# Kernel tuning notes

Hardware: AMD Instinct MI355X
Metric: run time of the kernel (lower is better)

## Reference

```python
import jax, jax.numpy as jnp
import numpy as np
from jax import lax

B, S, D = 8, 1024, 128

def setup_inputs() -> dict:
    key = jax.random.key(0)
    ks = jax.random.split(key, 6)
    scale = 1.0 / np.sqrt(D)
    return {
        "x": jax.random.normal(ks[0], (B, S, D), dtype=jnp.float32),
        "Wk": jax.random.normal(ks[1], (D, D), dtype=jnp.float32) * scale,
        "Wv": jax.random.normal(ks[2], (D, D), dtype=jnp.float32) * scale,
        "Wq": jax.random.normal(ks[3], (D, D), dtype=jnp.float32) * scale,
        "Wg": jax.random.normal(ks[4], (D, 3), dtype=jnp.float32) * scale,
        "bg": jnp.zeros((3,), dtype=jnp.float32),
    }

def reference(x, Wk, Wv, Wq, Wg, bg):
    b, s, d = x.shape
    k = x @ Wk  # [b,s,d]
    v = x @ Wv
    q = x @ Wq
    gates = jax.nn.sigmoid(x @ Wg + bg)  # [b,s,3]
    alpha, eta, theta = gates[..., 0], gates[..., 1], gates[..., 2]  # [b,s]

    M0 = jnp.zeros((b, d, d), dtype=x.dtype)
    S0 = jnp.zeros((b, d, d), dtype=x.dtype)

    # time-major scan inputs
    xs = (jnp.swapaxes(k, 0, 1), jnp.swapaxes(v, 0, 1), jnp.swapaxes(q, 0, 1),
          jnp.swapaxes(alpha, 0, 1), jnp.swapaxes(eta, 0, 1), jnp.swapaxes(theta, 0, 1))

    def scan_fn(carry, inp):
        M_prev, S_prev = carry
        kt, vt, qt, at, et, tt = inp  # kt/vt/qt: [b,d]; at/et/tt: [b]
        # NOTE: original einsum 'bd,bdd->bd' takes the DIAGONAL of M (faithful)
        diagM = jnp.einsum('bdd->bd', M_prev)  # [b,d]
        yt = qt * diagM
        pred = kt * diagM
        error = pred - vt
        grad = kt[:, :, None] * error[:, None, :]  # outer product [b,d,d]
        S_new = et[:, None, None] * S_prev - tt[:, None, None] * grad
        M_new = (1.0 - at[:, None, None]) * M_prev + S_new
        return (M_new, S_new), yt

    (M_final, S_final), outputs = lax.scan(scan_fn, (M0, S0), xs)
    outputs = jnp.swapaxes(outputs, 0, 1)  # [b,s,d]
    return (outputs, (M_final, S_final))
```

## Files before the change

### kernel.cpp

```cpp
#include <hip/hip_runtime.h>
#include <math.h>

#define NB 8
#define NS 1024
#define ND 128
#define NC 64
#define NL 16

#define OFF_K  0u
#define OFF_Q  1048576u
#define OFF_V  2097152u
#define OFF_E  3145728u
#define OFF_GA 4194304u
#define OFF_GE 4202496u
#define OFF_GT 4210688u
#define OFF_W  4218880u
#define OFF_C  4227072u
#define OFF_P  4235264u

#define PL_A00 (OFF_P)
#define PL_A01 (OFF_P +  65536u)
#define PL_A10 (OFF_P + 131072u)
#define PL_A11 (OFF_P + 196608u)
#define PL_B0  (OFF_P + 262144u)
#define PL_B1  (OFF_P + 327680u)
#define PL_MST (OFF_P + 393216u)
#define PL_SST (OFF_P + 458752u)
#define PL_WCA (OFF_P + 524288u)
#define PL_WCB (OFF_P + 524800u)
#define PL_WCD (OFF_P + 525312u)
#define PL_WRQ (OFF_P + 525824u)
#define PL_WRP (OFF_P + 526336u)
#define PL_WRA (OFF_P + 526848u)
#define OFF_WT (OFF_P + 532480u)
#define WT_LO  49152u

typedef short bf16x8 __attribute__((ext_vector_type(8)));
typedef float f32x4  __attribute__((ext_vector_type(4)));

static __device__ __forceinline__ unsigned short f2bf(float f) {
    unsigned u = __builtin_bit_cast(unsigned, f);
    unsigned r = (u + 0x7FFFu + ((u >> 16) & 1u)) >> 16;
    return (unsigned short)r;
}
static __device__ __forceinline__ float bf2f(unsigned short h) {
    unsigned u = ((unsigned)h) << 16;
    return __builtin_bit_cast(float, u);
}
static __device__ __forceinline__ void split2(float a, float b,
                                              unsigned& hi, unsigned& lo) {
    unsigned short ah = f2bf(a), bh = f2bf(b);
    float ar = a - bf2f(ah), br = b - bf2f(bh);
    hi = (unsigned)ah | ((unsigned)bh << 16);
    lo = (unsigned)f2bf(ar) | ((unsigned)f2bf(br) << 16);
}

__global__ __launch_bounds__(256) void wtprep_kernel(
    const float* __restrict__ Wk, const float* __restrict__ Wv,
    const float* __restrict__ Wq, unsigned short* __restrict__ wtg,
    float* __restrict__ outMS)
{
    const int m    = blockIdx.x >> 4;
    const int cgrp = blockIdx.x & 15;
    const int tid  = threadIdx.x;
    const int cl   = tid >> 5;
    const int h    = tid & 31;
    const int c    = cgrp * 8 + cl;
    const float* W = (m == 0) ? Wk : (m == 1) ? Wv : Wq;

    float f[4];
#pragma unroll
    for (int i = 0; i < 4; ++i)
        f[i] = W[(h * 4 + i) * ND + c];
    uint2 hi, lo;
    split2(f[0], f[1], hi.x, lo.x);
    split2(f[2], f[3], hi.y, lo.y);
    const unsigned base = (unsigned)m * 16384u + (unsigned)c * 128u + (unsigned)h * 4u;
    *(uint2*)&wtg[base]         = hi;
    *(uint2*)&wtg[WT_LO + base] = lo;

    const int gidx = blockIdx.x * 256 + tid;
    const float4 z = {0.f, 0.f, 0.f, 0.f};
#pragma unroll
    for (int l = 0; l < 6; ++l) {
        int i4 = gidx + l * 12288;
        if (i4 < 65536) ((float4*)outMS)[i4] = z;
    }
}

__global__ __launch_bounds__(256) void proj_mfma(
    const float* __restrict__ x, const unsigned short* __restrict__ wtg,
    const float* __restrict__ Wg, const float* __restrict__ bg,
    float* __restrict__ Kb, float* __restrict__ Vb, float* __restrict__ Qb,
    float* __restrict__ ga, float* __restrict__ ge, float* __restrict__ gt)
{
    __shared__ unsigned short xs_hi[32 * 136];
    __shared__ unsigned short xs_lo[32 * 136];
    __shared__ unsigned short wt_hi[64 * 136];
    __shared__ unsigned short wt_lo[64 * 136];

    const int tid  = threadIdx.x;
    const int bid  = blockIdx.x;
    const int m    = bid >> 9;
    const int rt   = (bid >> 1) & 255;
    const int ch   = bid & 1;
    const int row0 = rt * 32;

    const float4* x4 = (const float4*)x;
#pragma unroll
    for (int l = 0; l < 4; ++l) {
        int idx = tid + l * 256;
        int r = idx >> 5, kq = idx & 31;
        float4 f = x4[(row0 + r) * 32 + kq];
        uint2 hi, lo;
        split2(f.x, f.y, hi.x, lo.x);
        split2(f.z, f.w, hi.y, lo.y);
        *(uint2*)&xs_hi[r * 136 + kq * 4] = hi;
        *(uint2*)&xs_lo[r * 136 + kq * 4] = lo;
    }
    const uint4* wh4 = (const uint4*)(wtg + m * 16384 + ch * 64 * 128);
    const uint4* wl4 = (const uint4*)(wtg + WT_LO + m * 16384 + ch * 64 * 128);
#pragma unroll
    for (int l = 0; l < 4; ++l) {
        int idx = tid + l * 256;
        int c = idx >> 4, u = idx & 15;
        *(uint4*)&wt_hi[c * 136 + u * 8] = wh4[c * 16 + u];
        *(uint4*)&wt_lo[c * 136 + u * 8] = wl4[c * 16 + u];
    }
    __syncthreads();

    const int wid  = tid >> 6;
    const int lane = tid & 63;
    const int rg   = wid >> 1;
    const int cg   = wid & 1;
    const int lrow = rg * 16 + (lane & 15);
    const int quad = lane >> 4;

    f32x4 acc[2];
    acc[0] = (f32x4){0.f, 0.f, 0.f, 0.f};
    acc[1] = (f32x4){0.f, 0.f, 0.f, 0.f};

#pragma unroll
    for (int kk = 0; kk < 4; ++kk) {
        bf16x8 ah = *(const bf16x8*)&xs_hi[lrow * 136 + kk * 32 + quad * 8];
        bf16x8 al = *(const bf16x8*)&xs_lo[lrow * 136 + kk * 32 + quad * 8];
#pragma unroll
        for (int ct = 0; ct < 2; ++ct) {
            int cl = cg * 32 + ct * 16 + (lane & 15);
            bf16x8 bh = *(const bf16x8*)&wt_hi[cl * 136 + kk * 32 + quad * 8];
            bf16x8 bl = *(const bf16x8*)&wt_lo[cl * 136 + kk * 32 + quad * 8];
            acc[ct] = __builtin_amdgcn_mfma_f32_16x16x32_bf16(ah, bh, acc[ct], 0, 0, 0);
            acc[ct] = __builtin_amdgcn_mfma_f32_16x16x32_bf16(ah, bl, acc[ct], 0, 0, 0);
            acc[ct] = __builtin_amdgcn_mfma_f32_16x16x32_bf16(al, bh, acc[ct], 0, 0, 0);
        }
    }

    float* dst = (m == 0) ? Kb : (m == 1) ? Vb : Qb;
#pragma unroll
    for (int ct = 0; ct < 2; ++ct) {
        int ocol = ch * 64 + cg * 32 + ct * 16 + (lane & 15);
#pragma unroll
        for (int r4 = 0; r4 < 4; ++r4) {
            int orow = row0 + rg * 16 + quad * 4 + r4;
            dst[orow * ND + ocol] = acc[ct][r4];
        }
    }

    if (m == 0 && ch == 0 && tid < 96) {
        int r = tid / 3, j = tid % 3;
        float z = bg[j];
        const float* xr = x + (row0 + r) * ND;
#pragma unroll 4
        for (int i = 0; i < ND; ++i)
            z = fmaf(xr[i], Wg[i * 3 + j], z);
        float gate = 1.0f / (1.0f + expf(-z));
        int row = row0 + r;
        float* gd = (j == 0) ? ga : (j == 1) ? ge : gt;
        gd[row] = gate;
    }
}

__global__ __launch_bounds__(128) void scan_phase1(
    const float* __restrict__ Kb, const float* __restrict__ Vb,
    const float* __restrict__ ga, const float* __restrict__ ge,
    const float* __restrict__ gt, float* __restrict__ ws)
{
    __shared__ float la[NL], le[NL], lt[NL];
    const int tid = threadIdx.x;
    const int b   = blockIdx.x >> 6;
    const int c   = blockIdx.x & 63;
    const int t0  = c * NL;
    const int g0  = b * NS + t0;

    if (tid < 16)       la[tid]      = ga[g0 + tid];
    else if (tid < 32)  le[tid - 16] = ge[g0 + tid - 16];
    else if (tid < 48)  lt[tid - 32] = gt[g0 + tid - 32];
    __syncthreads();

    const int d = tid;
    float A00 = 1.f, A01 = 0.f, A10 = 0.f, A11 = 1.f, B0 = 0.f, B1 = 0.f;
    int base = g0 * ND + d;
#pragma unroll
    for (int t = 0; t < NL; ++t) {
        float k = Kb[base], v = Vb[base];
        float a = la[t], e = le[t], th = lt[t];
        float tk = th * k;
        float gg = -tk * k;
        float h  = tk * v;
        float p  = (1.0f - a) + gg;
        float u0 = e * A10;
        float u1 = e * A11;
        float u2 = fmaf(e, B1, h);
        float n00 = fmaf(p, A00, u0), n10 = fmaf(gg, A00, u0);
        float n01 = fmaf(p, A01, u1), n11 = fmaf(gg, A01, u1);
        float nb0 = fmaf(p, B0, u2),  nb1 = fmaf(gg, B0, u2);
        A00 = n00; A01 = n01; A10 = n10; A11 = n11; B0 = nb0; B1 = nb1;
        base += ND;
    }
    const int pidx = (b * NC + c) * ND + d;
    ws[PL_A00 + pidx] = A00;
    ws[PL_A01 + pidx] = A01;
    ws[PL_A10 + pidx] = A10;
    ws[PL_A11 + pidx] = A11;
    ws[PL_B0  + pidx] = B0;
    ws[PL_B1  + pidx] = B1;

    if (tid == 0) {
        float al = 1.f, be = 1.f, de = 0.f;
#pragma unroll
        for (int t = NL - 1; t >= 0; --t) {
            float e1 = le[t];
            float o1 = 1.0f - la[t];
            de = fmaf(e1, de, o1 * be);
            al *= e1;
            be *= o1;
        }
        ws[PL_WCA + b * NC + c] = al;
        ws[PL_WCB + b * NC + c] = be;
        ws[PL_WCD + b * NC + c] = de;
    }
}

__global__ __launch_bounds__(64) void scan_phase2(float* __restrict__ ws)
{
    const int tid = threadIdx.x;
    if (blockIdx.x < 16) {
        const int b = blockIdx.x >> 1;
        const int d = (blockIdx.x & 1) * 64 + tid;
        float m = 0.f, s = 0.f;
        int idx = (b * NC) * ND + d;
#pragma unroll 4
        for (int c = 0; c < NC; ++c) {
            ws[PL_MST + idx] = m;
            ws[PL_SST + idx] = s;
            float A00 = ws[PL_A00 + idx], A01 = ws[PL_A01 + idx];
            float A10 = ws[PL_A10 + idx], A11 = ws[PL_A11 + idx];
            float B0  = ws[PL_B0  + idx], B1  = ws[PL_B1  + idx];
            float nm = fmaf(A00, m, fmaf(A01, s, B0));
            float ns = fmaf(A10, m, fmaf(A11, s, B1));
            m = nm; s = ns;
            idx += ND;
        }
    } else if (tid < 8) {
        const int b = tid;
        float Qp = 1.f, P = 1.f, A = 1.f;
        for (int c = NC - 1; c >= 0; --c) {
            ws[PL_WRQ + b * NC + c] = Qp;
            ws[PL_WRP + b * NC + c] = P;
            ws[PL_WRA + b * NC + c] = A;
            float al = ws[PL_WCA + b * NC + c];
            float be = ws[PL_WCB + b * NC + c];
            float de = ws[PL_WCD + b * NC + c];
            float nA = fmaf(al, A, de * P);
            Qp *= al; P *= be; A = nA;
        }
    }
}

__global__ __launch_bounds__(128) void scan_phase3(
    const float* __restrict__ Kb, const float* __restrict__ Vb,
    const float* __restrict__ Qb,
    const float* __restrict__ ga, const float* __restrict__ ge,
    const float* __restrict__ gt,
    float* __restrict__ out, float* __restrict__ errb,
    float* __restrict__ wb,  float* __restrict__ cb,
    float* __restrict__ ws)
{
    __shared__ float la[NL], le[NL], lt[NL];
    const int tid = threadIdx.x;
    const int b   = blockIdx.x >> 6;
    const int c   = blockIdx.x & 63;
    const int t0  = c * NL;
    const int g0  = b * NS + t0;

    if (tid < 16)       la[tid]      = ga[g0 + tid];
    else if (tid < 32)  le[tid - 16] = ge[g0 + tid - 16];
    else if (tid < 48)  lt[tid - 32] = gt[g0 + tid - 32];
    __syncthreads();

    const int d = tid;
    const int pidx = (b * NC + c) * ND + d;
    float m = ws[PL_MST + pidx];
    float s = ws[PL_SST + pidx];
    int base = g0 * ND + d;
#pragma unroll
    for (int t = 0; t < NL; ++t) {
        float k = Kb[base], v = Vb[base], q = Qb[base];
        float a = la[t], e = le[t], th = lt[t];
        float err = fmaf(k, m, -v);
        out[base]  = q * m;
        errb[base] = err;
        float tk = th * k;
        float u  = fmaf(-(tk * k), m, tk * v);
        s = fmaf(e, s, u);
        m = fmaf(1.0f - a, m, s);
        base += ND;
    }

    if (tid == 0) {
        float Qp = ws[PL_WRQ + b * NC + c];
        float P  = ws[PL_WRP + b * NC + c];
        float A  = ws[PL_WRA + b * NC + c];
#pragma unroll
        for (int t = NL - 1; t >= 0; --t) {
            wb[g0 + t] = -lt[t] * Qp;
            cb[g0 + t] = -lt[t] * A;
            float e1 = le[t];
            float o1 = 1.0f - la[t];
            Qp *= e1;
            P  *= o1;
            A   = fmaf(e1, A, P);
        }
    }
}

__global__ __launch_bounds__(256) void finalgemm_kernel(
    const float* __restrict__ Kb, const float* __restrict__ errb,
    const float* __restrict__ wb, const float* __restrict__ cb,
    float* __restrict__ outMS)
{
    __shared__ float ks[64 * 16];
    __shared__ float wcs[64 * 2];
    const int tid = threadIdx.x;
    const int bid = blockIdx.x;
    const int b   = bid >> 7;
    const int tc  = (bid >> 3) & 15;
    const int rg  = bid & 7;
    const int bt0 = b * NS + tc * 64;

    {
        int tl = tid >> 2, r4 = tid & 3;
        *(float4*)&ks[tl * 16 + r4 * 4] =
            *(const float4*)&Kb[(bt0 + tl) * ND + rg * 16 + r4 * 4];
    }
    if (tid < 64) {
        wcs[tid * 2]     = wb[bt0 + tid];
        wcs[tid * 2 + 1] = cb[bt0 + tid];
    }
    __syncthreads();

    const int j = tid & 127;
    const int h = tid >> 7;
    float accM[8], accS[8];
#pragma unroll
    for (int i = 0; i < 8; ++i) { accM[i] = 0.f; accS[i] = 0.f; }

    int ebase = bt0 * ND + j;
#pragma unroll 4
    for (int t = 0; t < 64; ++t) {
        float ej = errb[ebase];
        float2 wc = *(const float2*)&wcs[t * 2];
        float wej = wc.x * ej, cej = wc.y * ej;
        float4 k0 = *(const float4*)&ks[t * 16 + h * 8];
        float4 k1 = *(const float4*)&ks[t * 16 + h * 8 + 4];
        accS[0] = fmaf(k0.x, wej, accS[0]); accM[0] = fmaf(k0.x, cej, accM[0]);
        accS[1] = fmaf(k0.y, wej, accS[1]); accM[1] = fmaf(k0.y, cej, accM[1]);
        accS[2] = fmaf(k0.z, wej, accS[2]); accM[2] = fmaf(k0.z, cej, accM[2]);
        accS[3] = fmaf(k0.w, wej, accS[3]); accM[3] = fmaf(k0.w, cej, accM[3]);
        accS[4] = fmaf(k1.x, wej, accS[4]); accM[4] = fmaf(k1.x, cej, accM[4]);
        accS[5] = fmaf(k1.y, wej, accS[5]); accM[5] = fmaf(k1.y, cej, accM[5]);
        accS[6] = fmaf(k1.z, wej, accS[6]); accM[6] = fmaf(k1.z, cej, accM[6]);
        accS[7] = fmaf(k1.w, wej, accS[7]); accM[7] = fmaf(k1.w, cej, accM[7]);
        ebase += ND;
    }

    const int robase = rg * 16 + h * 8;
#pragma unroll
    for (int i = 0; i < 8; ++i) {
        int off = b * (ND * ND) + (robase + i) * ND + j;
        atomicAdd(&outMS[off], accM[i]);
        atomicAdd(&outMS[131072u + off], accS[i]);
    }
}

extern "C" void kernel_launch(void* const* d_in, const int* in_sizes, int n_in,
                              void* d_out, int out_size, void* d_ws, size_t ws_size,
                              hipStream_t stream) {
    const float* x  = (const float*)d_in[0];
    const float* Wk = (const float*)d_in[1];
    const float* Wv = (const float*)d_in[2];
    const float* Wq = (const float*)d_in[3];
    const float* Wg = (const float*)d_in[4];
    const float* bg = (const float*)d_in[5];
    float* out = (float*)d_out;
    float* ws  = (float*)d_ws;

    float* Kb  = ws + OFF_K;
    float* Qb  = ws + OFF_Q;
    float* Vb  = ws + OFF_V;
    float* Eb  = ws + OFF_E;
    float* ga  = ws + OFF_GA;
    float* ge  = ws + OFF_GE;
    float* gt  = ws + OFF_GT;
    float* wbf = ws + OFF_W;
    float* cbf = ws + OFF_C;
    float* outMS = out + 1048576u;
    unsigned short* wtg = (unsigned short*)(ws + OFF_WT);

    wtprep_kernel<<<48, 256, 0, stream>>>(Wk, Wv, Wq, wtg, outMS);
    proj_mfma<<<1536, 256, 0, stream>>>(x, wtg, Wg, bg,
                                        Kb, Vb, Qb, ga, ge, gt);
    scan_phase1<<<NB * NC, 128, 0, stream>>>(Kb, Vb, ga, ge, gt, ws);
    scan_phase2<<<17, 64, 0, stream>>>(ws);
    scan_phase3<<<NB * NC, 128, 0, stream>>>(Kb, Vb, Qb, ga, ge, gt,
                                             out, Eb, wbf, cbf, ws);
    finalgemm_kernel<<<1024, 256, 0, stream>>>(Kb, Eb, wbf, cbf, outMS);
}
```

Before: 117.2 us.

## Fuse three scan phases into one cooperative kernel with grid syncs

Merges the chunk-summary, cross-chunk prefix, and chunk-replay scan kernels into a single cooperative launch separated by grid-wide syncs. K, V and Q for each chunk are loaded into registers once and reused in both the summary and replay passes, so the second global read is gone. This removes two kernel launches and the reload of K/V. In exchange it adds two grid barriers, and the middle phase runs on only 9 of 512 blocks while the others wait. The 48 extra registers per thread may also reduce occupancy.

Result: slower. 242.4 us (+106.8%).

```diff
diff --git a/kernel.cpp b/kernel.cpp
--- a/kernel.cpp
+++ b/kernel.cpp
@@ -1,5 +1,8 @@
 #include <hip/hip_runtime.h>
+#include <hip/hip_cooperative_groups.h>
 #include <math.h>
+
+namespace cg = cooperative_groups;
 
 #define NB 8
 #define NS 1024
@@ -180,11 +183,17 @@
     }
 }
 
-__global__ __launch_bounds__(128) void scan_phase1(
+__global__ __launch_bounds__(128) void scan_fused(
     const float* __restrict__ Kb, const float* __restrict__ Vb,
+    const float* __restrict__ Qb,
     const float* __restrict__ ga, const float* __restrict__ ge,
-    const float* __restrict__ gt, float* __restrict__ ws)
+    const float* __restrict__ gt,
+    float* __restrict__ out, float* __restrict__ errb,
+    float* __restrict__ wb,  float* __restrict__ cb,
+    float* __restrict__ ws)
 {
+    cg::grid_group grid = cg::this_grid();
+
     __shared__ float la[NL], le[NL], lt[NL];
     const int tid = threadIdx.x;
     const int b   = blockIdx.x >> 6;
@@ -195,62 +204,69 @@
     if (tid < 16)       la[tid]      = ga[g0 + tid];
     else if (tid < 32)  le[tid - 16] = ge[g0 + tid - 16];
     else if (tid < 48)  lt[tid - 32] = gt[g0 + tid - 32];
+
+    float k[NL], v[NL], q[NL];
+    {
+        int base = g0 * ND + tid;
+#pragma unroll
+        for (int t = 0; t < NL; ++t) {
+            k[t] = Kb[base];
+            v[t] = Vb[base];
+            q[t] = Qb[base];
+            base += ND;
+        }
+    }
     __syncthreads();
 
-    const int d = tid;
-    float A00 = 1.f, A01 = 0.f, A10 = 0.f, A11 = 1.f, B0 = 0.f, B1 = 0.f;
-    int base = g0 * ND + d;
-#pragma unroll
-    for (int t = 0; t < NL; ++t) {
-        float k = Kb[base], v = Vb[base];
-        float a = la[t], e = le[t], th = lt[t];
-        float tk = th * k;
-        float gg = -tk * k;
-        float h  = tk * v;
-        float p  = (1.0f - a) + gg;
-        float u0 = e * A10;
-        float u1 = e * A11;
-        float u2 = fmaf(e, B1, h);
-        float n00 = fmaf(p, A00, u0), n10 = fmaf(gg, A00, u0);
-        float n01 = fmaf(p, A01, u1), n11 = fmaf(gg, A01, u1);
-        float nb0 = fmaf(p, B0, u2),  nb1 = fmaf(gg, B0, u2);
-        A00 = n00; A01 = n01; A10 = n10; A11 = n11; B0 = nb0; B1 = nb1;
-        base += ND;
-    }
-    const int pidx = (b * NC + c) * ND + d;
-    ws[PL_A00 + pidx] = A00;
-    ws[PL_A01 + pidx] = A01;
-    ws[PL_A10 + pidx] = A10;
-    ws[PL_A11 + pidx] = A11;
-    ws[PL_B0  + pidx] = B0;
-    ws[PL_B1  + pidx] = B1;
-
-    if (tid == 0) {
-        float al = 1.f, be = 1.f, de = 0.f;
-#pragma unroll
-        for (int t = NL - 1; t >= 0; --t) {
-            float e1 = le[t];
-            float o1 = 1.0f - la[t];
-            de = fmaf(e1, de, o1 * be);
-            al *= e1;
-            be *= o1;
-        }
-        ws[PL_WCA + b * NC + c] = al;
-        ws[PL_WCB + b * NC + c] = be;
-        ws[PL_WCD + b * NC + c] = de;
-    }
-}
-
-__global__ __launch_bounds__(64) void scan_phase2(float* __restrict__ ws)
-{
-    const int tid = threadIdx.x;
-    if (blockIdx.x < 16) {
-        const int b = blockIdx.x >> 1;
-        const int d = (blockIdx.x & 1) * 64 + tid;
+    {
+        float A00 = 1.f, A01 = 0.f, A10 = 0.f, A11 = 1.f, B0 = 0.f, B1 = 0.f;
+#pragma unroll
+        for (int t = 0; t < NL; ++t) {
+            float a = la[t], e = le[t], th = lt[t];
+            float tk = th * k[t];
+            float gg = -tk * k[t];
+            float h  = tk * v[t];
+            float p  = (1.0f - a) + gg;
+            float u0 = e * A10;
+            float u1 = e * A11;
+            float u2 = fmaf(e, B1, h);
+            float n00 = fmaf(p, A00, u0), n10 = fmaf(gg, A00, u0);
+            float n01 = fmaf(p, A01, u1), n11 = fmaf(gg, A01, u1);
+            float nb0 = fmaf(p, B0, u2),  nb1 = fmaf(gg, B0, u2);
+            A00 = n00; A01 = n01; A10 = n10; A11 = n11; B0 = nb0; B1 = nb1;
+        }
+        const int pidx = (b * NC + c) * ND + tid;
+        ws[PL_A00 + pidx] = A00;
+        ws[PL_A01 + pidx] = A01;
+        ws[PL_A10 + pidx] = A10;
+        ws[PL_A11 + pidx] = A11;
+        ws[PL_B0  + pidx] = B0;
+        ws[PL_B1  + pidx] = B1;
+
+        if (tid == 0) {
+            float al = 1.f, be = 1.f, de = 0.f;
+#pragma unroll
+            for (int t = NL - 1; t >= 0; --t) {
+                float e1 = le[t];
+                float o1 = 1.0f - la[t];
+                de = fmaf(e1, de, o1 * be);
+                al *= e1;
+                be *= o1;
+            }
+            ws[PL_WCA + b * NC + c] = al;
+            ws[PL_WCB + b * NC + c] = be;
+            ws[PL_WCD + b * NC + c] = de;
+        }
+    }
+
+    grid.sync();
+
+    if (blockIdx.x < 8) {
+        const int pb = blockIdx.x;
         float m = 0.f, s = 0.f;
-        int idx = (b * NC) * ND + d;
+        int idx = (pb * NC) * ND + tid;
 #pragma unroll 4
-        for (int c = 0; c < NC; ++c) {
+        for (int cc = 0; cc < NC; ++cc) {
             ws[PL_MST + idx] = m;
             ws[PL_SST + idx] = s;
             float A00 = ws[PL_A00 + idx], A01 = ws[PL_A01 + idx];
@@ -261,75 +277,55 @@
             m = nm; s = ns;
             idx += ND;
         }
-    } else if (tid < 8) {
-        const int b = tid;
+    } else if (blockIdx.x == 8 && tid < 8) {
+        const int pb = tid;
         float Qp = 1.f, P = 1.f, A = 1.f;
-        for (int c = NC - 1; c >= 0; --c) {
-            ws[PL_WRQ + b * NC + c] = Qp;
-            ws[PL_WRP + b * NC + c] = P;
-            ws[PL_WRA + b * NC + c] = A;
-            float al = ws[PL_WCA + b * NC + c];
-            float be = ws[PL_WCB + b * NC + c];
-            float de = ws[PL_WCD + b * NC + c];
+        for (int cc = NC - 1; cc >= 0; --cc) {
+            ws[PL_WRQ + pb * NC + cc] = Qp;
+            ws[PL_WRP + pb * NC + cc] = P;
+            ws[PL_WRA + pb * NC + cc] = A;
+            float al = ws[PL_WCA + pb * NC + cc];
+            float be = ws[PL_WCB + pb * NC + cc];
+            float de = ws[PL_WCD + pb * NC + cc];
             float nA = fmaf(al, A, de * P);
             Qp *= al; P *= be; A = nA;
         }
     }
-}
-
-__global__ __launch_bounds__(128) void scan_phase3(
-    const float* __restrict__ Kb, const float* __restrict__ Vb,
-    const float* __restrict__ Qb,
-    const float* __restrict__ ga, const float* __restrict__ ge,
-    const float* __restrict__ gt,
-    float* __restrict__ out, float* __restrict__ errb,
-    float* __restrict__ wb,  float* __restrict__ cb,
-    float* __restrict__ ws)
-{
-    __shared__ float la[NL], le[NL], lt[NL];
-    const int tid = threadIdx.x;
-    const int b   = blockIdx.x >> 6;
-    const int c   = blockIdx.x & 63;
-    const int t0  = c * NL;
-    const int g0  = b * NS + t0;
-
-    if (tid < 16)       la[tid]      = ga[g0 + tid];
-    else if (tid < 32)  le[tid - 16] = ge[g0 + tid - 16];
-    else if (tid < 48)  lt[tid - 32] = gt[g0 + tid - 32];
-    __syncthreads();
-
-    const int d = tid;
-    const int pidx = (b * NC + c) * ND + d;
-    float m = ws[PL_MST + pidx];
-    float s = ws[PL_SST + pidx];
-    int base = g0 * ND + d;
-#pragma unroll
-    for (int t = 0; t < NL; ++t) {
-        float k = Kb[base], v = Vb[base], q = Qb[base];
-        float a = la[t], e = le[t], th = lt[t];
-        float err = fmaf(k, m, -v);
-        out[base]  = q * m;
-        errb[base] = err;
-        float tk = th * k;
-        float u  = fmaf(-(tk * k), m, tk * v);
-        s = fmaf(e, s, u);
-        m = fmaf(1.0f - a, m, s);
-        base += ND;
-    }
-
-    if (tid == 0) {
-        float Qp = ws[PL_WRQ + b * NC + c];
-        float P  = ws[PL_WRP + b * NC + c];
-        float A  = ws[PL_WRA + b * NC + c];
-#pragma unroll
-        for (int t = NL - 1; t >= 0; --t) {
-            wb[g0 + t] = -lt[t] * Qp;
-            cb[g0 + t] = -lt[t] * A;
-            float e1 = le[t];
-            float o1 = 1.0f - la[t];
-            Qp *= e1;
-            P  *= o1;
-            A   = fmaf(e1, A, P);
+
+    grid.sync();
+
+    {
+        const int pidx = (b * NC + c) * ND + tid;
+        float m = ws[PL_MST + pidx];
+        float s = ws[PL_SST + pidx];
+        int base = g0 * ND + tid;
+#pragma unroll
+        for (int t = 0; t < NL; ++t) {
+            float a = la[t], e = le[t], th = lt[t];
+            float err = fmaf(k[t], m, -v[t]);
+            out[base]  = q[t] * m;
+            errb[base] = err;
+            float tk = th * k[t];
+            float u  = fmaf(-(tk * k[t]), m, tk * v[t]);
+            s = fmaf(e, s, u);
+            m = fmaf(1.0f - a, m, s);
+            base += ND;
+        }
+
+        if (tid == 0) {
+            float Qp = ws[PL_WRQ + b * NC + c];
+            float P  = ws[PL_WRP + b * NC + c];
+            float A  = ws[PL_WRA + b * NC + c];
+#pragma unroll
+            for (int t = NL - 1; t >= 0; --t) {
+                wb[g0 + t] = -lt[t] * Qp;
+                cb[g0 + t] = -lt[t] * A;
+                float e1 = le[t];
+                float o1 = 1.0f - la[t];
+                Qp *= e1;
+                P  *= o1;
+                A   = fmaf(e1, A, P);
+            }
         }
     }
 }
@@ -420,9 +416,13 @@
     wtprep_kernel<<<48, 256, 0, stream>>>(Wk, Wv, Wq, wtg, outMS);
     proj_mfma<<<1536, 256, 0, stream>>>(x, wtg, Wg, bg,
                                         Kb, Vb, Qb, ga, ge, gt);
-    scan_phase1<<<NB * NC, 128, 0, stream>>>(Kb, Vb, ga, ge, gt, ws);
-    scan_phase2<<<17, 64, 0, stream>>>(ws);
-    scan_phase3<<<NB * NC, 128, 0, stream>>>(Kb, Vb, Qb, ga, ge, gt,
-                                             out, Eb, wbf, cbf, ws);
+
+    void* sargs[] = {(void*)&Kb, (void*)&Vb, (void*)&Qb,
+                     (void*)&ga, (void*)&ge, (void*)&gt,
+                     (void*)&out, (void*)&Eb, (void*)&wbf, (void*)&cbf,
+                     (void*)&ws};
+    hipLaunchCooperativeKernel((void*)scan_fused, dim3(NB * NC), dim3(128),
+                               sargs, 0, stream);
+
     finalgemm_kernel<<<1024, 256, 0, stream>>>(Kb, Eb, wbf, cbf, outMS);
 }
```
